# Kernel tuning notes

Measured on AMD Instinct MI355X. Metric: run time of the kernel, lower is better.

Reference implementation:

```python
import jax, jax.numpy as jnp
import numpy as np

STEPS = 10
HIDDEN = 16


def _lift_world(uv, depth, cam2world, intrinsics):
    # uv: [B,N,2], depth: [B,N], returns world coords [B,N,3]
    fx = intrinsics[:, 0, 0][:, None]
    fy = intrinsics[:, 1, 1][:, None]
    cx = intrinsics[:, 0, 2][:, None]
    cy = intrinsics[:, 1, 2][:, None]
    x_lift = (uv[:, :, 0] - cx) / fx * depth
    y_lift = (uv[:, :, 1] - cy) / fy * depth
    pts_hom = jnp.stack((x_lift, y_lift, depth, jnp.ones_like(depth)), axis=-1)  # [B,N,4]
    world = jnp.einsum('bij,bnj->bni', cam2world, pts_hom)[:, :, :3]
    return world


def reference(cam2world, intrinsics, uv, initial_depth,
              W_phi, b_phi, W_ih, b_ih, W_hh, b_hh, W_out, b_out):
    B, N, _ = uv.shape
    F = W_phi.shape[1]

    # ray directions through pixels (z_cam = 1 plane)
    pixel_pts = _lift_world(uv, jnp.ones((B, N), uv.dtype), cam2world, intrinsics)
    cam_pos = cam2world[:, :3, 3]
    ray_dirs = pixel_pts - cam_pos[:, None, :]
    ray_dirs = ray_dirs / jnp.linalg.norm(ray_dirs, axis=2, keepdims=True)

    world0 = _lift_world(uv, initial_depth[:, :, 0], cam2world, intrinsics)

    h0 = jnp.zeros((B * N, HIDDEN), world0.dtype)
    c0 = jnp.zeros((B * N, HIDDEN), world0.dtype)

    def step(carry, _):
        world, h, c = carry
        # phi: per-point feature net (stand-in: relu(Linear 3->F))
        v = jax.nn.relu(jnp.einsum('bnd,df->bnf', world, W_phi) + b_phi)
        x = v.reshape(B * N, F)
        gates = x @ W_ih.T + b_ih + h @ W_hh.T + b_hh  # [BN, 4H]
        i, f, g, o = jnp.split(gates, 4, axis=1)  # torch LSTMCell gate order
        c = jax.nn.sigmoid(f) * c + jax.nn.sigmoid(i) * jnp.tanh(g)
        h = jax.nn.sigmoid(o) * jnp.tanh(c)
        sd = (h @ W_out.T + b_out).reshape(B, N, 1)  # signed distance
        world = world + ray_dirs * sd
        return (world, h, c), None

    (world, _, _), _ = jax.lax.scan(step, (world0, h0, c0), None, length=STEPS)

    # final depth: camera-frame z of world points
    pts_hom = jnp.concatenate((world, jnp.ones((B, N, 1), world.dtype)), axis=2)
    c2w_inv = jnp.linalg.inv(cam2world)
    pts_cam = jnp.einsum('bij,bnj->bni', c2w_inv, pts_hom)
    depth = pts_cam[:, :, 2:3]
    return world, depth


def setup_inputs() -> dict:
    key = jax.random.key(0)
    ks = jax.random.split(key, 12)
    B, N, F = 8, 16384, 256
    H = HIDDEN

    # cam2world: proper-ish poses (orthonormal rotation via QR + translation)
    R = jnp.linalg.qr(jax.random.normal(ks[0], (B, 3, 3)))[0]
    t = jax.random.normal(ks[1], (B, 3)) * 2.0
    cam2world = jnp.zeros((B, 4, 4)).at[:, :3, :3].set(R).at[:, :3, 3].set(t).at[:, 3, 3].set(1.0)

    intrinsics = jnp.zeros((B, 3, 3))
    intrinsics = intrinsics.at[:, 0, 0].set(500.0).at[:, 1, 1].set(500.0)
    intrinsics = intrinsics.at[:, 0, 2].set(64.0).at[:, 1, 2].set(64.0).at[:, 2, 2].set(1.0)

    uv = jax.random.uniform(ks[2], (B, N, 2)) * 128.0  # pixel coords in a 128x128 image
    initial_depth = 0.05 + 0.0005 * jax.random.normal(ks[3], (B, N, 1))

    s = 1.0 / np.sqrt(F)
    return {
        'cam2world': cam2world.astype(jnp.float32),
        'intrinsics': intrinsics.astype(jnp.float32),
        'uv': uv.astype(jnp.float32),
        'initial_depth': initial_depth.astype(jnp.float32),
        'W_phi': jax.random.normal(ks[4], (3, F)) * 0.5,
        'b_phi': jax.random.normal(ks[5], (F,)) * 0.01,
        'W_ih': jax.random.normal(ks[6], (4 * H, F)) * s,
        'b_ih': jnp.zeros((4 * H,)).at[H:2 * H].set(1.0),  # forget-gate bias init
        'W_hh': jnp.linalg.qr(jax.random.normal(ks[7], (4 * H, H)))[0][:4 * H],
        'b_hh': jnp.zeros((4 * H,)),
        'W_out': jax.random.normal(ks[8], (1, H)) * (1.0 / np.sqrt(H)),
        'b_out': jnp.zeros((1,)),
    }
```

## Files before the change

kernel.cpp:

```cpp
#include <hip/hip_runtime.h>
#include <math.h>

#define FEAT 256
#define HID  16
#define GATES 64
#define STEPS 10

#define GPACK_N   (9*4*64*8)
#define PHIA_N    (8*64*8)
#define WS_PHIA_B 36864

typedef unsigned short ushort_t;
typedef __attribute__((ext_vector_type(8)))  short  short8;
typedef __attribute__((ext_vector_type(4)))  float  floatx4;
typedef __attribute__((ext_vector_type(16))) float  floatx16;
typedef __attribute__((ext_vector_type(2)))  unsigned int uint2v;
typedef __attribute__((ext_vector_type(4)))  unsigned int uintx4;

__device__ __forceinline__ ushort_t f2bf_bits(float f) {
    union { float f; unsigned u; } cv; cv.f = f;
    unsigned u = cv.u;
    u = (u + 0x7FFFu + ((u >> 16) & 1u)) >> 16;
    return (ushort_t)u;
}

__device__ __forceinline__ unsigned pk2bf(float lo, float hi) {
    unsigned r;
    asm("v_cvt_pk_bf16_f32 %0, %1, %2" : "=v"(r) : "v"(lo), "v"(hi));
    return r;
}

__device__ __forceinline__ unsigned relupk(float a, float b) {
    return pk2bf(fmaxf(a, 0.f), fmaxf(b, 0.f));
}

__device__ __forceinline__ unsigned packhl(float x) {
    unsigned u = __float_as_uint(x);
    float hi = __uint_as_float(u & 0xFFFF0000u);
    return pk2bf(hi, x - hi);
}

__global__ void prep(const float* __restrict__ Wphi, const float* __restrict__ bphi,
                     const float* __restrict__ Wih,  const float* __restrict__ bih,
                     const float* __restrict__ Whh,  const float* __restrict__ bhh,
                     void* __restrict__ ws) {
    int idx = blockIdx.x * 256 + threadIdx.x;
    const float L = 1.4426950408889634f;
    if (idx < GPACK_N) {
        int e    = idx & 7;
        int lane = (idx >> 3) & 63;
        int n    = (idx >> 9) & 3;
        int kc   = idx >> 11;
        int k    = kc * 32 + (lane >> 4) * 8 + e;
        int col  = n * 16 + (lane & 15);
        float v;
        if (k < FEAT) {
            v = Wih[col * FEAT + k];
        } else {
            int k2 = k - FEAT;
            if (k2 < HID)       v = Whh[col * HID + k2];
            else if (k2 == HID) v = bih[col] + bhh[col];
            else                v = 0.f;
        }
        float sc = (col >= 32 && col < 48) ? (2.f * L) : L;
        ((ushort_t*)ws)[idx] = f2bf_bits(v * sc);
    } else if (idx < GPACK_N + PHIA_N) {
        int j    = idx - GPACK_N;
        int e    = j & 7;
        int lane = (j >> 3) & 63;
        int ft   = j >> 9;
        int f    = ft * 32 + (lane & 31);
        float v = 0.f;
        if (lane < 32) {
            if (e < 6)       v = Wphi[(e >> 1) * FEAT + f];
            else if (e == 6) v = bphi[f];
        }
        ((ushort_t*)((char*)ws + WS_PHIA_B))[j] = f2bf_bits(v);
    }
}

__global__ __launch_bounds__(256, 2) void march(
    const float* __restrict__ c2w, const float* __restrict__ intr,
    const float* __restrict__ uv,  const float* __restrict__ dep0,
    const void* __restrict__ ws,   const float* __restrict__ Wout,
    const float* __restrict__ bout, float* __restrict__ out, int B, int N) {

    __shared__ __align__(16) ushort_t Blds[GPACK_N];
    __shared__ __align__(16) ushort_t Xlds[4][64][40];
    __shared__ __align__(16) ushort_t Hlds[4][64][40];
    __shared__ __align__(16) float    Sdls[4][64];

    int tid = threadIdx.x;
    int w = tid >> 6, l = tid & 63;
    int lc = l & 15, lg = l >> 4;
    int l31 = l & 31;
    bool hi32 = (l >= 32);
    int ray = blockIdx.x * 256 + tid;
    int BN = B * N;
    int b = ray / N;

    {
        const uintx4* src = (const uintx4*)ws;
        uintx4* dst = (uintx4*)Blds;
        for (int i = tid; i < GPACK_N / 8; i += 256) dst[i] = src[i];
    }

    short8 phiA[8];
    {
        const short8* pA = (const short8*)((const char*)ws + WS_PHIA_B);
#pragma unroll
        for (int ft = 0; ft < 8; ++ft) phiA[ft] = pA[ft * 64 + l];
    }

    const float* M = c2w + b * 16;
    float R00 = M[0], R01 = M[1], R02 = M[2], t0 = M[3];
    float R10 = M[4], R11 = M[5], R12 = M[6], t1 = M[7];
    float R20 = M[8], R21 = M[9], R22 = M[10], t2 = M[11];
    const float* Kc = intr + b * 9;
    float fx = Kc[0], cx = Kc[2], fy = Kc[4], cy = Kc[5];

    float u = uv[ray * 2 + 0];
    float v = uv[ray * 2 + 1];
    float d0 = dep0[ray];

    float xl = (u - cx) / fx;
    float yl = (v - cy) / fy;
    float dx = R00 * xl + R01 * yl + R02;
    float dy = R10 * xl + R11 * yl + R12;
    float dz = R20 * xl + R21 * yl + R22;
    float invn = rsqrtf(dx * dx + dy * dy + dz * dz);
    float rdx = dx * invn, rdy = dy * invn, rdz = dz * invn;
    float w0 = fmaf(dx, d0, t0);
    float w1 = fmaf(dy, d0, t1);
    float w2 = fmaf(dz, d0, t2);

    {
        uintx4 z4 = {0u, 0u, 0u, 0u};
        uintx4 o4 = {0x00003F80u, 0u, 0u, 0u};
        uintx4* hr = (uintx4*)&Hlds[w][l][0];
        hr[0] = z4; hr[1] = z4; hr[2] = o4; hr[3] = z4;
    }

    float wj = Wout[lc];
    float bo = bout[0];

    float h[HID], c[HID];
#pragma unroll
    for (int j = 0; j < HID; ++j) { h[j] = 0.f; c[j] = 0.f; }

    __syncthreads();

#pragma unroll 1
    for (int s = 0; s < STEPS; ++s) {
        float s0 = __shfl(w0, l31 + 32);
        float s1 = __shfl(w1, l31 + 32);
        float s2 = __shfl(w2, l31 + 32);
        short8 bw0, bw1;
        {
            unsigned a0 = hi32 ? 0u : packhl(w0);
            unsigned a1 = hi32 ? 0u : packhl(w1);
            unsigned a2 = hi32 ? 0u : packhl(w2);
            unsigned a3 = hi32 ? 0u : 0x00003F80u;
            unsigned c0 = hi32 ? 0u : packhl(s0);
            unsigned c1 = hi32 ? 0u : packhl(s1);
            unsigned c2 = hi32 ? 0u : packhl(s2);
            union { unsigned u[4]; short8 s; } cv0, cv1;
            cv0.u[0] = a0; cv0.u[1] = a1; cv0.u[2] = a2; cv0.u[3] = a3;
            cv1.u[0] = c0; cv1.u[1] = c1; cv1.u[2] = c2; cv1.u[3] = a3;
            bw0 = cv0.s; bw1 = cv1.s;
        }

        floatx4 acc[4][4];
#pragma unroll
        for (int m = 0; m < 4; ++m)
#pragma unroll
            for (int n = 0; n < 4; ++n) acc[m][n] = (floatx4){0.f, 0.f, 0.f, 0.f};

#pragma unroll
        for (int kc = 0; kc < 8; ++kc) {
            floatx16 zz = (floatx16){0.f,0.f,0.f,0.f,0.f,0.f,0.f,0.f,
                                     0.f,0.f,0.f,0.f,0.f,0.f,0.f,0.f};
            floatx16 p0 = __builtin_amdgcn_mfma_f32_32x32x16_bf16(phiA[kc], bw0, zz, 0, 0, 0);
            floatx16 p1 = __builtin_amdgcn_mfma_f32_32x32x16_bf16(phiA[kc], bw1, zz, 0, 0, 0);
            {
                uint2v* q0 = (uint2v*)&Xlds[w][l31][4 * (int)hi32];
                uint2v d;
                d.x = relupk(p0[0],  p0[1]);  d.y = relupk(p0[2],  p0[3]);  q0[0] = d;
                d.x = relupk(p0[4],  p0[5]);  d.y = relupk(p0[6],  p0[7]);  q0[2] = d;
                d.x = relupk(p0[8],  p0[9]);  d.y = relupk(p0[10], p0[11]); q0[4] = d;
                d.x = relupk(p0[12], p0[13]); d.y = relupk(p0[14], p0[15]); q0[6] = d;
                uint2v* q1 = (uint2v*)&Xlds[w][32 + l31][4 * (int)hi32];
                d.x = relupk(p1[0],  p1[1]);  d.y = relupk(p1[2],  p1[3]);  q1[0] = d;
                d.x = relupk(p1[4],  p1[5]);  d.y = relupk(p1[6],  p1[7]);  q1[2] = d;
                d.x = relupk(p1[8],  p1[9]);  d.y = relupk(p1[10], p1[11]); q1[4] = d;
                d.x = relupk(p1[12], p1[13]); d.y = relupk(p1[14], p1[15]); q1[6] = d;
            }
            short8 af[4], bf[4];
#pragma unroll
            for (int m = 0; m < 4; ++m)
                af[m] = *(const short8*)&Xlds[w][16 * m + lc][lg * 8];
#pragma unroll
            for (int n = 0; n < 4; ++n)
                bf[n] = *(const short8*)&Blds[((kc * 4 + n) * 64 + l) * 8];
#pragma unroll
            for (int m = 0; m < 4; ++m)
#pragma unroll
                for (int n = 0; n < 4; ++n)
                    acc[m][n] = __builtin_amdgcn_mfma_f32_16x16x32_bf16(
                        af[m], bf[n], acc[m][n], 0, 0, 0);
        }

        {
            short8 af[4], bf[4];
#pragma unroll
            for (int m = 0; m < 4; ++m)
                af[m] = *(const short8*)&Hlds[w][16 * m + lc][lg * 8];
#pragma unroll
            for (int n = 0; n < 4; ++n)
                bf[n] = *(const short8*)&Blds[((8 * 4 + n) * 64 + l) * 8];
#pragma unroll
            for (int m = 0; m < 4; ++m)
#pragma unroll
                for (int n = 0; n < 4; ++n)
                    acc[m][n] = __builtin_amdgcn_mfma_f32_16x16x32_bf16(
                        af[m], bf[n], acc[m][n], 0, 0, 0);
        }

        const float L2 = 2.8853900817779268f;
        float sp[4][4];
#pragma unroll
        for (int m = 0; m < 4; ++m) {
#pragma unroll
            for (int i = 0; i < 4; ++i) {
                float ig = __builtin_amdgcn_rcpf(1.f + __builtin_amdgcn_exp2f(-acc[m][0][i]));
                float fg = __builtin_amdgcn_rcpf(1.f + __builtin_amdgcn_exp2f(-acc[m][1][i]));
                float gg = fmaf(-2.f, __builtin_amdgcn_rcpf(1.f + __builtin_amdgcn_exp2f(acc[m][2][i])), 1.f);
                float og = __builtin_amdgcn_rcpf(1.f + __builtin_amdgcn_exp2f(-acc[m][3][i]));
                int idx = m * 4 + i;
                float cn = fmaf(fg, c[idx], ig * gg);
                c[idx] = cn;
                float tc = fmaf(-2.f, __builtin_amdgcn_rcpf(1.f + __builtin_amdgcn_exp2f(L2 * cn)), 1.f);
                float hn = og * tc;
                h[idx] = hn;
                sp[m][i] = hn * wj;
            }
        }
#pragma unroll
        for (int r = 1; r < 16; r <<= 1) {
#pragma unroll
            for (int m = 0; m < 4; ++m)
#pragma unroll
                for (int i = 0; i < 4; ++i)
                    sp[m][i] += __shfl_xor(sp[m][i], r, 64);
        }
        if (lc == 0) {
#pragma unroll
            for (int m = 0; m < 4; ++m) {
                floatx4 vv = {sp[m][0], sp[m][1], sp[m][2], sp[m][3]};
                *(floatx4*)&Sdls[w][16 * m + 4 * lg] = vv;
            }
        }
#pragma unroll
        for (int m = 0; m < 4; ++m)
#pragma unroll
            for (int i = 0; i < 4; ++i) {
                unsigned hb = pk2bf(h[m * 4 + i], h[m * 4 + i]);
                Hlds[w][16 * m + 4 * lg + i][lc] = (ushort_t)hb;
            }

        float sdv = Sdls[w][l] + bo;
        w0 = fmaf(rdx, sdv, w0);
        w1 = fmaf(rdy, sdv, w1);
        w2 = fmaf(rdz, sdv, w2);
    }

    int base = ray * 3;
    out[base + 0] = w0;
    out[base + 1] = w1;
    out[base + 2] = w2;
    float dd = R02 * (w0 - t0) + R12 * (w1 - t1) + R22 * (w2 - t2);
    out[BN * 3 + ray] = dd;
}

extern "C" void kernel_launch(void* const* d_in, const int* in_sizes, int n_in,
                              void* d_out, int out_size, void* d_ws, size_t ws_size,
                              hipStream_t stream) {
    const float* c2w  = (const float*)d_in[0];
    const float* intr = (const float*)d_in[1];
    const float* uv   = (const float*)d_in[2];
    const float* dep  = (const float*)d_in[3];
    const float* Wphi = (const float*)d_in[4];
    const float* bphi = (const float*)d_in[5];
    const float* Wih  = (const float*)d_in[6];
    const float* bih  = (const float*)d_in[7];
    const float* Whh  = (const float*)d_in[8];
    const float* bhh  = (const float*)d_in[9];
    const float* Wout = (const float*)d_in[10];
    const float* bout = (const float*)d_in[11];
    float* out = (float*)d_out;

    int B = in_sizes[0] / 16;
    int BN = in_sizes[3];
    int N = BN / B;
    int blocks = (BN + 255) / 256;

    int prep_items = GPACK_N + PHIA_N;
    prep<<<(prep_items + 255) / 256, 256, 0, stream>>>(Wphi, bphi, Wih, bih, Whh, bhh, d_ws);
    march<<<blocks, 256, 0, stream>>>(c2w, intr, uv, dep, d_ws, Wout, bout, out, B, N);
}
```

Before: 159.3 us.

## Fuse weight packing into march kernel and fold LSTM bias into accumulator init

Removes the separate prep kernel and has every march block pack the scaled bf16 gate weights and phi weights itself, reading straight from the fp32 inputs. The combined LSTM bias moves out of the packed constant-one column and into the accumulator initial value, which shrinks the hidden-state LDS row. The h register array is dropped so h values are written to LDS directly. This saves one kernel launch and its dependency, but each block now repeats roughly 18K strided global loads and conversions of weight data.

```diff
diff --git a/kernel.cpp b/kernel.cpp
--- a/kernel.cpp
+++ b/kernel.cpp
@@ -3,12 +3,8 @@
 
 #define FEAT 256
 #define HID  16
-#define GATES 64
 #define STEPS 10
-
-#define GPACK_N   (9*4*64*8)
-#define PHIA_N    (8*64*8)
-#define WS_PHIA_B 36864
+#define GPACK_N (9*4*64*8)
 
 typedef unsigned short ushort_t;
 typedef __attribute__((ext_vector_type(8)))  short  short8;
@@ -40,54 +36,18 @@
     return pk2bf(hi, x - hi);
 }
 
-__global__ void prep(const float* __restrict__ Wphi, const float* __restrict__ bphi,
-                     const float* __restrict__ Wih,  const float* __restrict__ bih,
-                     const float* __restrict__ Whh,  const float* __restrict__ bhh,
-                     void* __restrict__ ws) {
-    int idx = blockIdx.x * 256 + threadIdx.x;
-    const float L = 1.4426950408889634f;
-    if (idx < GPACK_N) {
-        int e    = idx & 7;
-        int lane = (idx >> 3) & 63;
-        int n    = (idx >> 9) & 3;
-        int kc   = idx >> 11;
-        int k    = kc * 32 + (lane >> 4) * 8 + e;
-        int col  = n * 16 + (lane & 15);
-        float v;
-        if (k < FEAT) {
-            v = Wih[col * FEAT + k];
-        } else {
-            int k2 = k - FEAT;
-            if (k2 < HID)       v = Whh[col * HID + k2];
-            else if (k2 == HID) v = bih[col] + bhh[col];
-            else                v = 0.f;
-        }
-        float sc = (col >= 32 && col < 48) ? (2.f * L) : L;
-        ((ushort_t*)ws)[idx] = f2bf_bits(v * sc);
-    } else if (idx < GPACK_N + PHIA_N) {
-        int j    = idx - GPACK_N;
-        int e    = j & 7;
-        int lane = (j >> 3) & 63;
-        int ft   = j >> 9;
-        int f    = ft * 32 + (lane & 31);
-        float v = 0.f;
-        if (lane < 32) {
-            if (e < 6)       v = Wphi[(e >> 1) * FEAT + f];
-            else if (e == 6) v = bphi[f];
-        }
-        ((ushort_t*)((char*)ws + WS_PHIA_B))[j] = f2bf_bits(v);
-    }
-}
-
 __global__ __launch_bounds__(256, 2) void march(
     const float* __restrict__ c2w, const float* __restrict__ intr,
     const float* __restrict__ uv,  const float* __restrict__ dep0,
-    const void* __restrict__ ws,   const float* __restrict__ Wout,
-    const float* __restrict__ bout, float* __restrict__ out, int B, int N) {
+    const float* __restrict__ Wphi, const float* __restrict__ bphi,
+    const float* __restrict__ Wih,  const float* __restrict__ bih,
+    const float* __restrict__ Whh,  const float* __restrict__ bhh,
+    const float* __restrict__ Wout, const float* __restrict__ bout,
+    float* __restrict__ out, int B, int N) {
 
     __shared__ __align__(16) ushort_t Blds[GPACK_N];
     __shared__ __align__(16) ushort_t Xlds[4][64][40];
-    __shared__ __align__(16) ushort_t Hlds[4][64][40];
+    __shared__ __align__(16) ushort_t Hlds[4][64][24];
     __shared__ __align__(16) float    Sdls[4][64];
 
     int tid = threadIdx.x;
@@ -99,18 +59,45 @@
     int BN = B * N;
     int b = ray / N;
 
-    {
-        const uintx4* src = (const uintx4*)ws;
-        uintx4* dst = (uintx4*)Blds;
-        for (int i = tid; i < GPACK_N / 8; i += 256) dst[i] = src[i];
+    const float L = 1.4426950408889634f;
+
+    for (int idx = tid; idx < GPACK_N; idx += 256) {
+        int e    = idx & 7;
+        int lane = (idx >> 3) & 63;
+        int n    = (idx >> 9) & 3;
+        int kc   = idx >> 11;
+        int k    = kc * 32 + (lane >> 4) * 8 + e;
+        int col  = n * 16 + (lane & 15);
+        float v = 0.f;
+        if (k < FEAT)                 v = Wih[col * FEAT + k];
+        else if (k - FEAT < HID)      v = Whh[col * HID + (k - FEAT)];
+        float sc = (col >= 32 && col < 48) ? (2.f * L) : L;
+        Blds[idx] = f2bf_bits(v * sc);
     }
 
     short8 phiA[8];
-    {
-        const short8* pA = (const short8*)((const char*)ws + WS_PHIA_B);
-#pragma unroll
-        for (int ft = 0; ft < 8; ++ft) phiA[ft] = pA[ft * 64 + l];
-    }
+#pragma unroll
+    for (int ft = 0; ft < 8; ++ft) {
+        float q0 = 0.f, q1 = 0.f, q2 = 0.f, q3 = 0.f;
+        if (!hi32) {
+            int f = ft * 32 + l31;
+            q0 = Wphi[f]; q1 = Wphi[FEAT + f]; q2 = Wphi[2 * FEAT + f]; q3 = bphi[f];
+        }
+        union { unsigned u[4]; short8 s; } cv;
+        cv.u[0] = pk2bf(q0, q0); cv.u[1] = pk2bf(q1, q1);
+        cv.u[2] = pk2bf(q2, q2); cv.u[3] = pk2bf(q3, 0.f);
+        phiA[ft] = cv.s;
+    }
+
+    float gbv[4];
+#pragma unroll
+    for (int n = 0; n < 4; ++n) {
+        int col = n * 16 + lc;
+        float sc = (n == 2) ? (2.f * L) : L;
+        gbv[n] = sc * (bih[col] + bhh[col]);
+    }
+    float wj = Wout[lc];
+    float bo = bout[0];
 
     const float* M = c2w + b * 16;
     float R00 = M[0], R01 = M[1], R02 = M[2], t0 = M[3];
@@ -136,17 +123,15 @@
 
     {
         uintx4 z4 = {0u, 0u, 0u, 0u};
-        uintx4 o4 = {0x00003F80u, 0u, 0u, 0u};
         uintx4* hr = (uintx4*)&Hlds[w][l][0];
-        hr[0] = z4; hr[1] = z4; hr[2] = o4; hr[3] = z4;
-    }
-
-    float wj = Wout[lc];
-    float bo = bout[0];
-
-    float h[HID], c[HID];
-#pragma unroll
-    for (int j = 0; j < HID; ++j) { h[j] = 0.f; c[j] = 0.f; }
+        hr[0] = z4; hr[1] = z4; hr[2] = z4;
+    }
+
+    short8 z8 = {0, 0, 0, 0, 0, 0, 0, 0};
+
+    float cst[HID];
+#pragma unroll
+    for (int j = 0; j < HID; ++j) cst[j] = 0.f;
 
     __syncthreads();
 
@@ -174,7 +159,8 @@
 #pragma unroll
         for (int m = 0; m < 4; ++m)
 #pragma unroll
-            for (int n = 0; n < 4; ++n) acc[m][n] = (floatx4){0.f, 0.f, 0.f, 0.f};
+            for (int n = 0; n < 4; ++n)
+                acc[m][n] = (floatx4){gbv[n], gbv[n], gbv[n], gbv[n]};
 
 #pragma unroll
         for (int kc = 0; kc < 8; ++kc) {
@@ -211,19 +197,19 @@
         }
 
         {
-            short8 af[4], bf[4];
-#pragma unroll
-            for (int m = 0; m < 4; ++m)
-                af[m] = *(const short8*)&Hlds[w][16 * m + lc][lg * 8];
+            short8 af[4], bf8[4];
+#pragma unroll
+            for (int m = 0; m < 4; ++m)
+                af[m] = (lg < 2) ? *(const short8*)&Hlds[w][16 * m + lc][8 * lg] : z8;
 #pragma unroll
             for (int n = 0; n < 4; ++n)
-                bf[n] = *(const short8*)&Blds[((8 * 4 + n) * 64 + l) * 8];
+                bf8[n] = *(const short8*)&Blds[((32 + n) * 64 + l) * 8];
 #pragma unroll
             for (int m = 0; m < 4; ++m)
 #pragma unroll
                 for (int n = 0; n < 4; ++n)
                     acc[m][n] = __builtin_amdgcn_mfma_f32_16x16x32_bf16(
-                        af[m], bf[n], acc[m][n], 0, 0, 0);
+                        af[m], bf8[n], acc[m][n], 0, 0, 0);
         }
 
         const float L2 = 2.8853900817779268f;
@@ -237,11 +223,11 @@
                 float gg = fmaf(-2.f, __builtin_amdgcn_rcpf(1.f + __builtin_amdgcn_exp2f(acc[m][2][i])), 1.f);
                 float og = __builtin_amdgcn_rcpf(1.f + __builtin_amdgcn_exp2f(-acc[m][3][i]));
                 int idx = m * 4 + i;
-                float cn = fmaf(fg, c[idx], ig * gg);
-                c[idx] = cn;
+                float cn = fmaf(fg, cst[idx], ig * gg);
+                cst[idx] = cn;
                 float tc = fmaf(-2.f, __builtin_amdgcn_rcpf(1.f + __builtin_amdgcn_exp2f(L2 * cn)), 1.f);
                 float hn = og * tc;
-                h[idx] = hn;
+                Hlds[w][16 * m + 4 * lg + i][lc] = (ushort_t)pk2bf(hn, hn);
                 sp[m][i] = hn * wj;
             }
         }
@@ -260,13 +246,6 @@
                 *(floatx4*)&Sdls[w][16 * m + 4 * lg] = vv;
             }
         }
-#pragma unroll
-        for (int m = 0; m < 4; ++m)
-#pragma unroll
-            for (int i = 0; i < 4; ++i) {
-                unsigned hb = pk2bf(h[m * 4 + i], h[m * 4 + i]);
-                Hlds[w][16 * m + 4 * lg + i][lc] = (ushort_t)hb;
-            }
 
         float sdv = Sdls[w][l] + bo;
         w0 = fmaf(rdx, sdv, w0);
@@ -304,7 +283,7 @@
     int N = BN / B;
     int blocks = (BN + 255) / 256;
 
-    int prep_items = GPACK_N + PHIA_N;
-    prep<<<(prep_items + 255) / 256, 256, 0, stream>>>(Wphi, bphi, Wih, bih, Whh, bhh, d_ws);
-    march<<<blocks, 256, 0, stream>>>(c2w, intr, uv, dep, d_ws, Wout, bout, out, B, N);
-}
+    march<<<blocks, 256, 0, stream>>>(c2w, intr, uv, dep,
+                                      Wphi, bphi, Wih, bih, Whh, bhh, Wout, bout,
+                                      out, B, N);
+}
```

New measurement: 177.5 us. 11.4% more time.
